# Kernel optimization log

Hardware: AMD Instinct MI355X
Metric: run time of the kernel (lower is better)

Reference implementation:

```python
import jax, jax.numpy as jnp
import numpy as np

# 3D PGA grade slices over the 16-component multivector (contiguous in standard basis order)
GRADE_SLICES = [(0, 1), (1, 5), (5, 11), (11, 15), (15, 16)]
GRADE_DIMS = [1, 4, 6, 4, 1]


def setup_inputs() -> dict:
    key = jax.random.key(0)
    ks = jax.random.split(key, 11)
    x = jax.random.normal(ks[0], (8, 2048, 128, 16), dtype=jnp.float32)
    inp = {"x": x}
    for g, d in enumerate(GRADE_DIMS):
        # match nn.Linear default init scale ~ U(-1/sqrt(d), 1/sqrt(d)); randn is fine for a numeric baseline
        inp[f"w{g}"] = jax.random.normal(ks[1 + 2 * g], (d, d), dtype=jnp.float32) / np.sqrt(d)
        inp[f"b{g}"] = jax.random.normal(ks[2 + 2 * g], (d,), dtype=jnp.float32) / np.sqrt(d)
    return inp


def reference(x, w0, b0, w1, b1, w2, b2, w3, b3, w4, b4):
    ws = [w0, w1, w2, w3, w4]
    bs = [b0, b1, b2, b3, b4]
    # Block-diagonal per-grade linear: gather slice, y = x_g @ W_g^T + b_g, scatter back.
    # Since grade index sets are contiguous, scatter == concatenate along last dim.
    outs = []
    for (lo, hi), w, b in zip(GRADE_SLICES, ws, bs):
        xg = x[..., lo:hi]                       # [..., d_g]
        outs.append(jnp.einsum("...i,oi->...o", xg, w) + b)
    return jnp.concatenate(outs, axis=-1)        # [..., 16]
```

## Files before the change

kernel.cpp:

```cpp
#include <hip/hip_runtime.h>


__global__ __launch_bounds__(256) void GradeWiseLinear_kernel(
    const float* __restrict__ x,
    const float* __restrict__ w0, const float* __restrict__ b0,
    const float* __restrict__ w1, const float* __restrict__ b1,
    const float* __restrict__ w2, const float* __restrict__ b2,
    const float* __restrict__ w3, const float* __restrict__ b3,
    const float* __restrict__ w4, const float* __restrict__ b4,
    float* __restrict__ out, int n4)
{
    __shared__ float s[86];
    {
        int t = threadIdx.x;
        if (t < 86) {
            float v;
            if      (t == 0)  v = w0[0];
            else if (t < 17)  v = w1[t - 1];
            else if (t < 53)  v = w2[t - 17];
            else if (t < 69)  v = w3[t - 53];
            else if (t == 69) v = w4[0];
            else if (t == 70) v = b0[0];
            else if (t < 75)  v = b1[t - 71];
            else if (t < 81)  v = b2[t - 75];
            else if (t < 85)  v = b3[t - 81];
            else              v = b4[0];
            s[t] = v;
        }
    }
    __syncthreads();

    int g = blockIdx.x * 256 + threadIdx.x;
    if (g >= n4) return;

    const int j = g & 3;
    const float4* x4 = (const float4*)x;

    float4 me = x4[g];
    float4 up = x4[g - (int)(j > 0)];
    float4 dn = x4[g + (int)(j < 3)];

    float o0, o1, o2, o3;

    if (j == 0) {
        o0 = s[70] + me.x * s[0];
        o1 = s[71] + me.y * s[1] + me.z * s[2]  + me.w * s[3]  + dn.x * s[4];
        o2 = s[72] + me.y * s[5] + me.z * s[6]  + me.w * s[7]  + dn.x * s[8];
        o3 = s[73] + me.y * s[9] + me.z * s[10] + me.w * s[11] + dn.x * s[12];
    } else if (j == 1) {
        o0 = s[74] + up.y * s[13] + up.z * s[14] + up.w * s[15] + me.x * s[16];
        o1 = s[75] + me.y * s[17] + me.z * s[18] + me.w * s[19]
                   + dn.x * s[20] + dn.y * s[21] + dn.z * s[22];
        o2 = s[76] + me.y * s[23] + me.z * s[24] + me.w * s[25]
                   + dn.x * s[26] + dn.y * s[27] + dn.z * s[28];
        o3 = s[77] + me.y * s[29] + me.z * s[30] + me.w * s[31]
                   + dn.x * s[32] + dn.y * s[33] + dn.z * s[34];
    } else if (j == 2) {
        o0 = s[78] + up.y * s[35] + up.z * s[36] + up.w * s[37]
                   + me.x * s[38] + me.y * s[39] + me.z * s[40];
        o1 = s[79] + up.y * s[41] + up.z * s[42] + up.w * s[43]
                   + me.x * s[44] + me.y * s[45] + me.z * s[46];
        o2 = s[80] + up.y * s[47] + up.z * s[48] + up.w * s[49]
                   + me.x * s[50] + me.y * s[51] + me.z * s[52];
        o3 = s[81] + me.w * s[53] + dn.x * s[54] + dn.y * s[55] + dn.z * s[56];
    } else {
        o0 = s[82] + up.w * s[57] + me.x * s[58] + me.y * s[59] + me.z * s[60];
        o1 = s[83] + up.w * s[61] + me.x * s[62] + me.y * s[63] + me.z * s[64];
        o2 = s[84] + up.w * s[65] + me.x * s[66] + me.y * s[67] + me.z * s[68];
        o3 = s[85] + me.w * s[69];
    }

    ((float4*)out)[g] = make_float4(o0, o1, o2, o3);
}

extern "C" void kernel_launch(void* const* d_in, const int* in_sizes, int n_in,
                              void* d_out, int out_size, void* d_ws, size_t ws_size,
                              hipStream_t stream) {
    const float* x  = (const float*)d_in[0];
    const float* w0 = (const float*)d_in[1];
    const float* b0 = (const float*)d_in[2];
    const float* w1 = (const float*)d_in[3];
    const float* b1 = (const float*)d_in[4];
    const float* w2 = (const float*)d_in[5];
    const float* b2 = (const float*)d_in[6];
    const float* w3 = (const float*)d_in[7];
    const float* b3 = (const float*)d_in[8];
    const float* w4 = (const float*)d_in[9];
    const float* b4 = (const float*)d_in[10];
    float* out = (float*)d_out;

    int n4 = in_sizes[0] / 4;
    int block = 256;
    int grid = (n4 + block - 1) / block;

    GradeWiseLinear_kernel<<<grid, block, 0, stream>>>(
        x, w0, b0, w1, b1, w2, b2, w3, b3, w4, b4, out, n4);
}
```

Measured before the change: 243.9 us.

## Process one full 16-float multivector per thread instead of one float4

Each thread now loads all four float4s of a multivector row and computes all 16 outputs, replacing the previous scheme where each thread handled one float4 and reloaded neighbouring float4s plus branched on its lane position. This removes the three-fold redundant loads and the intra-wave divergence across the four cases. In exchange, per-thread global accesses are strided by 64 bytes, which lowers coalescing per instruction, and there are four times fewer threads.

```diff
diff --git a/kernel.cpp b/kernel.cpp
--- a/kernel.cpp
+++ b/kernel.cpp
@@ -8,7 +8,7 @@
     const float* __restrict__ w2, const float* __restrict__ b2,
     const float* __restrict__ w3, const float* __restrict__ b3,
     const float* __restrict__ w4, const float* __restrict__ b4,
-    float* __restrict__ out, int n4)
+    float* __restrict__ out, int nrows)
 {
     __shared__ float s[86];
     {
@@ -30,47 +30,51 @@
     }
     __syncthreads();
 
-    int g = blockIdx.x * 256 + threadIdx.x;
-    if (g >= n4) return;
+    int r = blockIdx.x * 256 + threadIdx.x;
+    if (r >= nrows) return;
 
-    const int j = g & 3;
-    const float4* x4 = (const float4*)x;
+    const float4* __restrict__ x4 = (const float4*)x;
+    float4* __restrict__ o4 = (float4*)out;
+    const int base = r * 4;
 
-    float4 me = x4[g];
-    float4 up = x4[g - (int)(j > 0)];
-    float4 dn = x4[g + (int)(j < 3)];
+    float4 a = x4[base + 0];
+    float4 p = x4[base + 1];
+    float4 c = x4[base + 2];
+    float4 d = x4[base + 3];
 
-    float o0, o1, o2, o3;
+    float4 y0, y1, y2, y3;
 
-    if (j == 0) {
-        o0 = s[70] + me.x * s[0];
-        o1 = s[71] + me.y * s[1] + me.z * s[2]  + me.w * s[3]  + dn.x * s[4];
-        o2 = s[72] + me.y * s[5] + me.z * s[6]  + me.w * s[7]  + dn.x * s[8];
-        o3 = s[73] + me.y * s[9] + me.z * s[10] + me.w * s[11] + dn.x * s[12];
-    } else if (j == 1) {
-        o0 = s[74] + up.y * s[13] + up.z * s[14] + up.w * s[15] + me.x * s[16];
-        o1 = s[75] + me.y * s[17] + me.z * s[18] + me.w * s[19]
-                   + dn.x * s[20] + dn.y * s[21] + dn.z * s[22];
-        o2 = s[76] + me.y * s[23] + me.z * s[24] + me.w * s[25]
-                   + dn.x * s[26] + dn.y * s[27] + dn.z * s[28];
-        o3 = s[77] + me.y * s[29] + me.z * s[30] + me.w * s[31]
-                   + dn.x * s[32] + dn.y * s[33] + dn.z * s[34];
-    } else if (j == 2) {
-        o0 = s[78] + up.y * s[35] + up.z * s[36] + up.w * s[37]
-                   + me.x * s[38] + me.y * s[39] + me.z * s[40];
-        o1 = s[79] + up.y * s[41] + up.z * s[42] + up.w * s[43]
-                   + me.x * s[44] + me.y * s[45] + me.z * s[46];
-        o2 = s[80] + up.y * s[47] + up.z * s[48] + up.w * s[49]
-                   + me.x * s[50] + me.y * s[51] + me.z * s[52];
-        o3 = s[81] + me.w * s[53] + dn.x * s[54] + dn.y * s[55] + dn.z * s[56];
-    } else {
-        o0 = s[82] + up.w * s[57] + me.x * s[58] + me.y * s[59] + me.z * s[60];
-        o1 = s[83] + up.w * s[61] + me.x * s[62] + me.y * s[63] + me.z * s[64];
-        o2 = s[84] + up.w * s[65] + me.x * s[66] + me.y * s[67] + me.z * s[68];
-        o3 = s[85] + me.w * s[69];
-    }
+    y0.x = s[70] + s[0] * a.x;
 
-    ((float4*)out)[g] = make_float4(o0, o1, o2, o3);
+    y0.y = s[71] + s[1]  * a.y + s[2]  * a.z + s[3]  * a.w + s[4]  * p.x;
+    y0.z = s[72] + s[5]  * a.y + s[6]  * a.z + s[7]  * a.w + s[8]  * p.x;
+    y0.w = s[73] + s[9]  * a.y + s[10] * a.z + s[11] * a.w + s[12] * p.x;
+    y1.x = s[74] + s[13] * a.y + s[14] * a.z + s[15] * a.w + s[16] * p.x;
+
+    y1.y = s[75] + s[17] * p.y + s[18] * p.z + s[19] * p.w
+                 + s[20] * c.x + s[21] * c.y + s[22] * c.z;
+    y1.z = s[76] + s[23] * p.y + s[24] * p.z + s[25] * p.w
+                 + s[26] * c.x + s[27] * c.y + s[28] * c.z;
+    y1.w = s[77] + s[29] * p.y + s[30] * p.z + s[31] * p.w
+                 + s[32] * c.x + s[33] * c.y + s[34] * c.z;
+    y2.x = s[78] + s[35] * p.y + s[36] * p.z + s[37] * p.w
+                 + s[38] * c.x + s[39] * c.y + s[40] * c.z;
+    y2.y = s[79] + s[41] * p.y + s[42] * p.z + s[43] * p.w
+                 + s[44] * c.x + s[45] * c.y + s[46] * c.z;
+    y2.z = s[80] + s[47] * p.y + s[48] * p.z + s[49] * p.w
+                 + s[50] * c.x + s[51] * c.y + s[52] * c.z;
+
+    y2.w = s[81] + s[53] * c.w + s[54] * d.x + s[55] * d.y + s[56] * d.z;
+    y3.x = s[82] + s[57] * c.w + s[58] * d.x + s[59] * d.y + s[60] * d.z;
+    y3.y = s[83] + s[61] * c.w + s[62] * d.x + s[63] * d.y + s[64] * d.z;
+    y3.z = s[84] + s[65] * c.w + s[66] * d.x + s[67] * d.y + s[68] * d.z;
+
+    y3.w = s[85] + s[69] * d.w;
+
+    o4[base + 0] = y0;
+    o4[base + 1] = y1;
+    o4[base + 2] = y2;
+    o4[base + 3] = y3;
 }
 
 extern "C" void kernel_launch(void* const* d_in, const int* in_sizes, int n_in,
@@ -89,10 +93,10 @@
     const float* b4 = (const float*)d_in[10];
     float* out = (float*)d_out;
 
-    int n4 = in_sizes[0] / 4;
+    int nrows = in_sizes[0] / 16;
     int block = 256;
-    int grid = (n4 + block - 1) / block;
+    int grid = (nrows + block - 1) / block;
 
     GradeWiseLinear_kernel<<<grid, block, 0, stream>>>(
-        x, w0, b0, w1, b1, w2, b2, w3, b3, w4, b4, out, n4);
+        x, w0, b0, w1, b1, w2, b2, w3, b3, w4, b4, out, nrows);
 }
```

Measured after the change: 252.8 us. +3.6%, slower.

## Replace neighbor loads with lane shuffles and use prefetching grid-stride loop

Applied to the files above, without the earlier changes.

Each thread now loads only its own float4 and gets the neighbouring components of its 16-wide multivector through cross-lane xor shuffles, instead of issuing two extra overlapping global loads. The launch is capped at 2048 blocks and each thread walks a grid-stride loop, prefetching its next float4 before computing the current one. This cuts redundant load instructions and block launch overhead, but lowers the number of resident blocks and relies on uniform lane activity for the shuffles.

```diff
diff --git a/kernel.cpp b/kernel.cpp
--- a/kernel.cpp
+++ b/kernel.cpp
@@ -30,47 +30,66 @@
     }
     __syncthreads();
 
+    const int stride = gridDim.x * 256;
     int g = blockIdx.x * 256 + threadIdx.x;
     if (g >= n4) return;
 
     const int j = g & 3;
-    const float4* x4 = (const float4*)x;
+    const float4* __restrict__ x4 = (const float4*)x;
+    float4* __restrict__ o4 = (float4*)out;
 
-    float4 me = x4[g];
-    float4 up = x4[g - (int)(j > 0)];
-    float4 dn = x4[g + (int)(j < 3)];
+    float4 cur = x4[g];
+    for (;;) {
+        int gn = g + stride;
+        bool have_next = (gn < n4);
+        float4 nxt;
+        if (have_next) nxt = x4[gn];
 
-    float o0, o1, o2, o3;
+        float4 e1, e3;
+        e1.x = __shfl_xor(cur.x, 1);
+        e1.y = __shfl_xor(cur.y, 1);
+        e1.z = __shfl_xor(cur.z, 1);
+        e1.w = __shfl_xor(cur.w, 1);
+        e3.x = __shfl_xor(cur.x, 3);
+        e3.y = __shfl_xor(cur.y, 3);
+        e3.z = __shfl_xor(cur.z, 3);
+        e3.w = __shfl_xor(cur.w, 3);
 
-    if (j == 0) {
-        o0 = s[70] + me.x * s[0];
-        o1 = s[71] + me.y * s[1] + me.z * s[2]  + me.w * s[3]  + dn.x * s[4];
-        o2 = s[72] + me.y * s[5] + me.z * s[6]  + me.w * s[7]  + dn.x * s[8];
-        o3 = s[73] + me.y * s[9] + me.z * s[10] + me.w * s[11] + dn.x * s[12];
-    } else if (j == 1) {
-        o0 = s[74] + up.y * s[13] + up.z * s[14] + up.w * s[15] + me.x * s[16];
-        o1 = s[75] + me.y * s[17] + me.z * s[18] + me.w * s[19]
-                   + dn.x * s[20] + dn.y * s[21] + dn.z * s[22];
-        o2 = s[76] + me.y * s[23] + me.z * s[24] + me.w * s[25]
-                   + dn.x * s[26] + dn.y * s[27] + dn.z * s[28];
-        o3 = s[77] + me.y * s[29] + me.z * s[30] + me.w * s[31]
-                   + dn.x * s[32] + dn.y * s[33] + dn.z * s[34];
-    } else if (j == 2) {
-        o0 = s[78] + up.y * s[35] + up.z * s[36] + up.w * s[37]
-                   + me.x * s[38] + me.y * s[39] + me.z * s[40];
-        o1 = s[79] + up.y * s[41] + up.z * s[42] + up.w * s[43]
-                   + me.x * s[44] + me.y * s[45] + me.z * s[46];
-        o2 = s[80] + up.y * s[47] + up.z * s[48] + up.w * s[49]
-                   + me.x * s[50] + me.y * s[51] + me.z * s[52];
-        o3 = s[81] + me.w * s[53] + dn.x * s[54] + dn.y * s[55] + dn.z * s[56];
-    } else {
-        o0 = s[82] + up.w * s[57] + me.x * s[58] + me.y * s[59] + me.z * s[60];
-        o1 = s[83] + up.w * s[61] + me.x * s[62] + me.y * s[63] + me.z * s[64];
-        o2 = s[84] + up.w * s[65] + me.x * s[66] + me.y * s[67] + me.z * s[68];
-        o3 = s[85] + me.w * s[69];
+        float4 y;
+        if (j == 0) {
+            y.x = s[70] + s[0]  * cur.x;
+            y.y = s[71] + s[1]  * cur.y + s[2]  * cur.z + s[3]  * cur.w + s[4]  * e1.x;
+            y.z = s[72] + s[5]  * cur.y + s[6]  * cur.z + s[7]  * cur.w + s[8]  * e1.x;
+            y.w = s[73] + s[9]  * cur.y + s[10] * cur.z + s[11] * cur.w + s[12] * e1.x;
+        } else if (j == 1) {
+            y.x = s[74] + s[13] * e1.y  + s[14] * e1.z  + s[15] * e1.w  + s[16] * cur.x;
+            y.y = s[75] + s[17] * cur.y + s[18] * cur.z + s[19] * cur.w
+                        + s[20] * e3.x  + s[21] * e3.y  + s[22] * e3.z;
+            y.z = s[76] + s[23] * cur.y + s[24] * cur.z + s[25] * cur.w
+                        + s[26] * e3.x  + s[27] * e3.y  + s[28] * e3.z;
+            y.w = s[77] + s[29] * cur.y + s[30] * cur.z + s[31] * cur.w
+                        + s[32] * e3.x  + s[33] * e3.y  + s[34] * e3.z;
+        } else if (j == 2) {
+            y.x = s[78] + s[35] * e3.y  + s[36] * e3.z  + s[37] * e3.w
+                        + s[38] * cur.x + s[39] * cur.y + s[40] * cur.z;
+            y.y = s[79] + s[41] * e3.y  + s[42] * e3.z  + s[43] * e3.w
+                        + s[44] * cur.x + s[45] * cur.y + s[46] * cur.z;
+            y.z = s[80] + s[47] * e3.y  + s[48] * e3.z  + s[49] * e3.w
+                        + s[50] * cur.x + s[51] * cur.y + s[52] * cur.z;
+            y.w = s[81] + s[53] * cur.w + s[54] * e1.x  + s[55] * e1.y  + s[56] * e1.z;
+        } else {
+            y.x = s[82] + s[57] * e1.w + s[58] * cur.x + s[59] * cur.y + s[60] * cur.z;
+            y.y = s[83] + s[61] * e1.w + s[62] * cur.x + s[63] * cur.y + s[64] * cur.z;
+            y.z = s[84] + s[65] * e1.w + s[66] * cur.x + s[67] * cur.y + s[68] * cur.z;
+            y.w = s[85] + s[69] * cur.w;
+        }
+
+        o4[g] = y;
+
+        if (!have_next) break;
+        cur = nxt;
+        g = gn;
     }
-
-    ((float4*)out)[g] = make_float4(o0, o1, o2, o3);
 }
 
 extern "C" void kernel_launch(void* const* d_in, const int* in_sizes, int n_in,
@@ -92,6 +111,7 @@
     int n4 = in_sizes[0] / 4;
     int block = 256;
     int grid = (n4 + block - 1) / block;
+    if (grid > 2048) grid = 2048;
 
     GradeWiseLinear_kernel<<<grid, block, 0, stream>>>(
         x, w0, b0, w1, b1, w2, b2, w3, b3, w4, b4, out, n4);
```

Measured after the change: 246.7 us. No clear change (+1.1%).
